# Optimization experiments

Hardware: AMD Instinct MI355X
Metric: run time of the kernel (lower is better)

Reference implementation:

```python
import jax, jax.numpy as jnp
import numpy as np

D_MODEL = 1024
NUM_HEADS = 16
HEAD_DIM = D_MODEL // NUM_HEADS


def setup_inputs() -> dict:
    key = jax.random.key(0)
    k_x, k_qkv, k_o = jax.random.split(key, 3)
    B, L = 2, 2048
    x = jax.random.normal(k_x, (B, L, D_MODEL), dtype=jnp.float32)
    # torch Linear weight [out, in]; y = x @ W.T. Scale ~ kaiming-uniform-ish.
    s = 1.0 / np.sqrt(D_MODEL)
    W_qkv = jax.random.uniform(k_qkv, (3 * D_MODEL, D_MODEL), dtype=jnp.float32, minval=-s, maxval=s)
    W_o = jax.random.uniform(k_o, (D_MODEL, D_MODEL), dtype=jnp.float32, minval=-s, maxval=s)
    return {"x": x, "W_qkv": W_qkv, "W_o": W_o}


def reference(x, W_qkv, W_o):
    B, L, D = x.shape
    H, dk = NUM_HEADS, HEAD_DIM
    qkv = (x @ W_qkv.T).reshape(B, L, 3, H, dk)
    q = qkv[:, :, 0].transpose(0, 2, 1, 3)  # [B,H,L,dk]
    k = qkv[:, :, 1].transpose(0, 2, 1, 3)
    v = qkv[:, :, 2].transpose(0, 2, 1, 3)
    scale = 1.0 / np.sqrt(dk).astype(np.float32)
    attn = jnp.einsum('bhqd,bhkd->bhqk', q, k) * scale  # [B,H,L,L]
    causal = jnp.tril(jnp.ones((L, L), dtype=bool))
    attn = jnp.where(causal, attn, -jnp.inf)
    attn = jax.nn.softmax(attn, axis=-1)
    y = jnp.einsum('bhqk,bhkd->bhqd', attn, v)  # [B,H,L,dk]
    y = y.transpose(0, 2, 1, 3).reshape(B, L, D)
    return y @ W_o.T
```

## Files before the change

kernel.cpp:

```cpp
#include <hip/hip_runtime.h>

typedef unsigned short u16;
typedef unsigned int   u32;

typedef __attribute__((ext_vector_type(4))) float  f32x4;
typedef __attribute__((ext_vector_type(8))) __bf16 bf16x8;

#define B_  2
#define L_  2048
#define H_  16

__device__ static inline u16 f2bf(float f) {
  u32 u = __builtin_bit_cast(u32, f);
  u32 r = u + 0x7fffu + ((u >> 16) & 1u);
  return (u16)(r >> 16);
}

__device__ static inline void gload_lds16(const u16* g, u16* lds) {
  __builtin_amdgcn_global_load_lds((__attribute__((address_space(1))) void*)(g),
                                   (__attribute__((address_space(3))) void*)(lds),
                                   16, 0, 0);
}

__global__ __launch_bounds__(256) void cvt3_kernel(
    const float4* __restrict__ a, uint2* __restrict__ ao, int na,
    const float4* __restrict__ b, uint2* __restrict__ bo, int nb,
    const float4* __restrict__ c, uint2* __restrict__ co, int nc)
{
  const int step = gridDim.x * 256;
  for (int i = blockIdx.x * 256 + threadIdx.x; i < na; i += step) {
    float4 f = a[i];
    ao[i] = make_uint2((u32)f2bf(f.x) | ((u32)f2bf(f.y) << 16),
                       (u32)f2bf(f.z) | ((u32)f2bf(f.w) << 16));
  }
  for (int i = blockIdx.x * 256 + threadIdx.x; i < nb; i += step) {
    float4 f = b[i];
    bo[i] = make_uint2((u32)f2bf(f.x) | ((u32)f2bf(f.y) << 16),
                       (u32)f2bf(f.z) | ((u32)f2bf(f.w) << 16));
  }
  for (int i = blockIdx.x * 256 + threadIdx.x; i < nc; i += step) {
    float4 f = c[i];
    co[i] = make_uint2((u32)f2bf(f.x) | ((u32)f2bf(f.y) << 16),
                       (u32)f2bf(f.z) | ((u32)f2bf(f.w) << 16));
  }
}

template <bool OUT_F32>
__global__ __launch_bounds__(256) void gemm_bt_kernel(
    const u16* __restrict__ A, const u16* __restrict__ Bt, void* __restrict__ Cv,
    const int K, const int N)
{
  __shared__ __attribute__((aligned(16))) u16 Al[128 * 64];
  __shared__ __attribute__((aligned(16))) u16 Bl[128 * 64];

  const int tid  = threadIdx.x;
  const int w    = tid >> 6;
  const int lane = tid & 63;
  const int m0 = blockIdx.y * 128;
  const int n0 = blockIdx.x * 128;
  const int mo = (w >> 1) * 64;
  const int no = (w & 1) * 64;

  const int srow = w * 32 + (lane >> 3);
  const int scol = (((lane & 7) ^ ((lane >> 3) & 7)) * 8);

  const f32x4 zero = {0.f, 0.f, 0.f, 0.f};
  f32x4 acc[4][4];
  #pragma unroll
  for (int i = 0; i < 4; ++i)
    #pragma unroll
    for (int j = 0; j < 4; ++j) acc[i][j] = zero;

  const int frow = lane & 15;
  const int fg   = lane >> 4;

  for (int k0 = 0; k0 < K; k0 += 64) {
    __syncthreads();
    #pragma unroll
    for (int inst = 0; inst < 4; ++inst) {
      const int r = srow + inst * 8;
      gload_lds16(A  + (size_t)(m0 + r) * K + k0 + scol, &Al[(w * 32 + inst * 8) * 64]);
      gload_lds16(Bt + (size_t)(n0 + r) * K + k0 + scol, &Bl[(w * 32 + inst * 8) * 64]);
    }
    __syncthreads();
    #pragma unroll
    for (int ks = 0; ks < 2; ++ks) {
      const int fco = ((ks * 4 + fg) ^ (frow & 7)) * 8;
      bf16x8 af[4], bfr[4];
      #pragma unroll
      for (int i = 0; i < 4; ++i)
        af[i] = *(const bf16x8*)&Al[(mo + i * 16 + frow) * 64 + fco];
      #pragma unroll
      for (int j = 0; j < 4; ++j)
        bfr[j] = *(const bf16x8*)&Bl[(no + j * 16 + frow) * 64 + fco];
      #pragma unroll
      for (int i = 0; i < 4; ++i)
        #pragma unroll
        for (int j = 0; j < 4; ++j)
          acc[i][j] = __builtin_amdgcn_mfma_f32_16x16x32_bf16(af[i], bfr[j], acc[i][j], 0, 0, 0);
    }
  }

  const int crow0 = m0 + mo + (lane >> 4) * 4;
  const int ccol0 = n0 + no + (lane & 15);
  #pragma unroll
  for (int i = 0; i < 4; ++i)
    #pragma unroll
    for (int j = 0; j < 4; ++j)
      #pragma unroll
      for (int r = 0; r < 4; ++r) {
        const size_t idx = (size_t)(crow0 + i * 16 + r) * N + (ccol0 + j * 16);
        if (OUT_F32) ((float*)Cv)[idx] = acc[i][j][r];
        else         ((u16*)Cv)[idx]   = f2bf(acc[i][j][r]);
      }
}

__global__ __launch_bounds__(256) void attn_mfma_kernel(const u16* __restrict__ qkv,
                                                        u16* __restrict__ y)
{
  __shared__ __attribute__((aligned(16))) u16 Kt[2][64 * 64];
  __shared__ __attribute__((aligned(16))) u16 Vt[2][64 * 72];
  __shared__ __attribute__((aligned(16))) u16 Pt[4][16 * 72];

  const int tid  = threadIdx.x;
  const int w    = tid >> 6;
  const int lane = tid & 63;
  const int fr   = lane & 15;
  const int fg   = lane >> 4;
  const int bh   = blockIdx.x;
  const int pi   = blockIdx.y;
  const int bb   = bh >> 4;
  const int hh   = bh & 15;
  const size_t rb = (size_t)bb * L_;

  const int vkk  = tid >> 2;
  const int vdb  = (tid & 3) * 16;
  const int vcol = vkk ^ ((tid & 3) * 16);

  const int pswz = (fr & 12) << 2;
  const int pfo0 = fr * 72 + ((fg * 8) ^ pswz);
  const int pfo1 = fr * 72 + ((32 + fg * 8) ^ pswz);

  const int ksr = w * 16 + (lane >> 3);
  const int ksc = (((lane & 7) ^ ((lane >> 3) & 7)) * 8);

  const int kco0 = ((fg) ^ (fr & 7)) * 8;
  const int kco1 = ((4 + fg) ^ (fr & 7)) * 8;

  const f32x4 zero = {0.f, 0.f, 0.f, 0.f};

  for (int pass = 0; pass < 2; ++pass) {
    const int qt = pass ? (31 - pi) : pi;
    const int q0 = qt * 64;
    const int qw = q0 + w * 16;

    const bf16x8 qf0 = *(const bf16x8*)(qkv + (rb + qw + fr) * 3072 + hh * 64 + fg * 8);
    const bf16x8 qf1 = *(const bf16x8*)(qkv + (rb + qw + fr) * 3072 + hh * 64 + 32 + fg * 8);

    f32x4 oacc[4];
    #pragma unroll
    for (int nt = 0; nt < 4; ++nt) oacc[nt] = zero;
    f32x4 lsum = zero;

    __syncthreads();
    #pragma unroll
    for (int inst = 0; inst < 2; ++inst)
      gload_lds16(qkv + (rb + 0 + ksr + inst * 8) * 3072 + 1024 + hh * 64 + ksc,
                  &Kt[0][(w * 16 + inst * 8) * 64]);
    {
      const u16* vp = qkv + (rb + 0 + vkk) * 3072 + 2048 + hh * 64 + vdb;
      uint4 a = *(const uint4*)vp;
      uint4 b = *(const uint4*)(vp + 8);
      u16 vals[16];
      *(uint4*)(vals)     = a;
      *(uint4*)(vals + 8) = b;
      #pragma unroll
      for (int i = 0; i < 16; ++i) Vt[0][(vdb + i) * 72 + vcol] = vals[i];
    }

    int cur = 0;
    for (int kt = 0; kt <= q0; kt += 64) {
      __syncthreads();

      const bool havenext = (kt + 64 <= q0);
      uint4 va, vb;
      if (havenext) {
        #pragma unroll
        for (int inst = 0; inst < 2; ++inst)
          gload_lds16(qkv + (rb + kt + 64 + ksr + inst * 8) * 3072 + 1024 + hh * 64 + ksc,
                      &Kt[cur ^ 1][(w * 16 + inst * 8) * 64]);
        const u16* vp = qkv + (rb + kt + 64 + vkk) * 3072 + 2048 + hh * 64 + vdb;
        va = *(const uint4*)vp;
        vb = *(const uint4*)(vp + 8);
      }

      f32x4 sacc[4];
      #pragma unroll
      for (int nt = 0; nt < 4; ++nt) sacc[nt] = zero;
      #pragma unroll
      for (int nt = 0; nt < 4; ++nt) {
        bf16x8 kf0 = *(const bf16x8*)&Kt[cur][(nt * 16 + fr) * 64 + kco0];
        sacc[nt] = __builtin_amdgcn_mfma_f32_16x16x32_bf16(qf0, kf0, sacc[nt], 0, 0, 0);
        bf16x8 kf1 = *(const bf16x8*)&Kt[cur][(nt * 16 + fr) * 64 + kco1];
        sacc[nt] = __builtin_amdgcn_mfma_f32_16x16x32_bf16(qf1, kf1, sacc[nt], 0, 0, 0);
      }

      if (kt == q0) {
        #pragma unroll
        for (int nt = 0; nt < 4; ++nt)
          #pragma unroll
          for (int r = 0; r < 4; ++r) {
            float p = (kt + nt * 16 + fr > qw + fg * 4 + r)
                          ? 0.f : __expf(sacc[nt][r] * 0.125f);
            lsum[r] += p;
            Pt[w][(fg * 4 + r) * 72 + ((nt * 16 + fr) ^ (fg * 16))] = f2bf(p);
          }
      } else {
        #pragma unroll
        for (int nt = 0; nt < 4; ++nt)
          #pragma unroll
          for (int r = 0; r < 4; ++r) {
            float p = __expf(sacc[nt][r] * 0.125f);
            lsum[r] += p;
            Pt[w][(fg * 4 + r) * 72 + ((nt * 16 + fr) ^ (fg * 16))] = f2bf(p);
          }
      }

      #pragma unroll
      for (int ks = 0; ks < 2; ++ks) {
        bf16x8 pf = *(const bf16x8*)&Pt[w][ks ? pfo1 : pfo0];
        #pragma unroll
        for (int nt = 0; nt < 4; ++nt) {
          bf16x8 vf = *(const bf16x8*)&Vt[cur][(nt * 16 + fr) * 72 + ((ks * 32 + fg * 8) ^ (nt * 16))];
          oacc[nt] = __builtin_amdgcn_mfma_f32_16x16x32_bf16(pf, vf, oacc[nt], 0, 0, 0);
        }
      }

      if (havenext) {
        u16 vals[16];
        *(uint4*)(vals)     = va;
        *(uint4*)(vals + 8) = vb;
        #pragma unroll
        for (int i = 0; i < 16; ++i) Vt[cur ^ 1][(vdb + i) * 72 + vcol] = vals[i];
      }
      cur ^= 1;
    }

    #pragma unroll
    for (int r = 0; r < 4; ++r) {
      float v = lsum[r];
      v += __shfl_xor(v, 1);
      v += __shfl_xor(v, 2);
      v += __shfl_xor(v, 4);
      v += __shfl_xor(v, 8);
      lsum[r] = 1.f / v;
    }

    #pragma unroll
    for (int nt = 0; nt < 4; ++nt)
      #pragma unroll
      for (int r = 0; r < 4; ++r)
        y[(rb + qw + fg * 4 + r) * 1024 + hh * 64 + nt * 16 + fr] =
            f2bf(oacc[nt][r] * lsum[r]);
  }
}

extern "C" void kernel_launch(void* const* d_in, const int* in_sizes, int n_in,
                              void* d_out, int out_size, void* d_ws, size_t ws_size,
                              hipStream_t stream)
{
  const float* x    = (const float*)d_in[0];
  const float* Wqkv = (const float*)d_in[1];
  const float* Wo   = (const float*)d_in[2];
  float* out = (float*)d_out;

  u16* xb    = (u16*)d_ws;
  u16* Wqkvb = xb    + (size_t)4096 * 1024;
  u16* Wob   = Wqkvb + (size_t)3072 * 1024;
  u16* qkv   = Wob   + (size_t)1024 * 1024;
  u16* y     = qkv   + (size_t)4096 * 3072;

  cvt3_kernel<<<dim3(2048), dim3(256), 0, stream>>>(
      (const float4*)x,    (uint2*)xb,    4096 * 1024 / 4,
      (const float4*)Wqkv, (uint2*)Wqkvb, 3072 * 1024 / 4,
      (const float4*)Wo,   (uint2*)Wob,   1024 * 1024 / 4);

  gemm_bt_kernel<false><<<dim3(3072 / 128, 4096 / 128), dim3(256), 0, stream>>>(
      xb, Wqkvb, qkv, 1024, 3072);
  attn_mfma_kernel<<<dim3(B_ * H_, 16), dim3(256), 0, stream>>>(qkv, y);
  gemm_bt_kernel<true><<<dim3(1024 / 128, 4096 / 128), dim3(256), 0, stream>>>(
      y, Wob, out, 1024, 1024);
}
```

Measured before the change: 185.1 us.

## Double-buffer GEMM LDS tiles and transpose attention MFMA layout for packed stores

The GEMM kernel now double-buffers its A/B LDS tiles, prefetching the next K-slice while computing the current one and dropping one barrier per iteration. The attention kernel swaps MFMA operand order so scores and outputs come out transposed. This lets P be written as packed 64-bit bf16 pairs, V be staged as packed key-pair dwords with a swizzle, the row sum be reduced with two shuffles instead of four per row, and the output be stored as vectorized 8-byte writes. The cost is doubled GEMM LDS use, which may lower occupancy.

Measured after the change: 188.7 us. Within noise of the previous version (+2.0%).

```diff
diff --git a/kernel.cpp b/kernel.cpp
--- a/kernel.cpp
+++ b/kernel.cpp
@@ -15,6 +15,9 @@
   u32 r = u + 0x7fffu + ((u >> 16) & 1u);
   return (u16)(r >> 16);
 }
+__device__ static inline u32 pack2(float a, float b) {
+  return (u32)f2bf(a) | ((u32)f2bf(b) << 16);
+}
 
 __device__ static inline void gload_lds16(const u16* g, u16* lds) {
   __builtin_amdgcn_global_load_lds((__attribute__((address_space(1))) void*)(g),
@@ -30,18 +33,15 @@
   const int step = gridDim.x * 256;
   for (int i = blockIdx.x * 256 + threadIdx.x; i < na; i += step) {
     float4 f = a[i];
-    ao[i] = make_uint2((u32)f2bf(f.x) | ((u32)f2bf(f.y) << 16),
-                       (u32)f2bf(f.z) | ((u32)f2bf(f.w) << 16));
+    ao[i] = make_uint2(pack2(f.x, f.y), pack2(f.z, f.w));
   }
   for (int i = blockIdx.x * 256 + threadIdx.x; i < nb; i += step) {
     float4 f = b[i];
-    bo[i] = make_uint2((u32)f2bf(f.x) | ((u32)f2bf(f.y) << 16),
-                       (u32)f2bf(f.z) | ((u32)f2bf(f.w) << 16));
+    bo[i] = make_uint2(pack2(f.x, f.y), pack2(f.z, f.w));
   }
   for (int i = blockIdx.x * 256 + threadIdx.x; i < nc; i += step) {
     float4 f = c[i];
-    co[i] = make_uint2((u32)f2bf(f.x) | ((u32)f2bf(f.y) << 16),
-                       (u32)f2bf(f.z) | ((u32)f2bf(f.w) << 16));
+    co[i] = make_uint2(pack2(f.x, f.y), pack2(f.z, f.w));
   }
 }
 
@@ -50,8 +50,8 @@
     const u16* __restrict__ A, const u16* __restrict__ Bt, void* __restrict__ Cv,
     const int K, const int N)
 {
-  __shared__ __attribute__((aligned(16))) u16 Al[128 * 64];
-  __shared__ __attribute__((aligned(16))) u16 Bl[128 * 64];
+  __shared__ __attribute__((aligned(16))) u16 Al[2][128 * 64];
+  __shared__ __attribute__((aligned(16))) u16 Bl[2][128 * 64];
 
   const int tid  = threadIdx.x;
   const int w    = tid >> 6;
@@ -74,31 +74,41 @@
   const int frow = lane & 15;
   const int fg   = lane >> 4;
 
+  #pragma unroll
+  for (int inst = 0; inst < 4; ++inst) {
+    const int r = srow + inst * 8;
+    gload_lds16(A  + (size_t)(m0 + r) * K + scol, &Al[0][(w * 32 + inst * 8) * 64]);
+    gload_lds16(Bt + (size_t)(n0 + r) * K + scol, &Bl[0][(w * 32 + inst * 8) * 64]);
+  }
+
+  int cur = 0;
   for (int k0 = 0; k0 < K; k0 += 64) {
     __syncthreads();
-    #pragma unroll
-    for (int inst = 0; inst < 4; ++inst) {
-      const int r = srow + inst * 8;
-      gload_lds16(A  + (size_t)(m0 + r) * K + k0 + scol, &Al[(w * 32 + inst * 8) * 64]);
-      gload_lds16(Bt + (size_t)(n0 + r) * K + k0 + scol, &Bl[(w * 32 + inst * 8) * 64]);
-    }
-    __syncthreads();
+    if (k0 + 64 < K) {
+      #pragma unroll
+      for (int inst = 0; inst < 4; ++inst) {
+        const int r = srow + inst * 8;
+        gload_lds16(A  + (size_t)(m0 + r) * K + k0 + 64 + scol, &Al[cur ^ 1][(w * 32 + inst * 8) * 64]);
+        gload_lds16(Bt + (size_t)(n0 + r) * K + k0 + 64 + scol, &Bl[cur ^ 1][(w * 32 + inst * 8) * 64]);
+      }
+    }
     #pragma unroll
     for (int ks = 0; ks < 2; ++ks) {
       const int fco = ((ks * 4 + fg) ^ (frow & 7)) * 8;
       bf16x8 af[4], bfr[4];
       #pragma unroll
       for (int i = 0; i < 4; ++i)
-        af[i] = *(const bf16x8*)&Al[(mo + i * 16 + frow) * 64 + fco];
+        af[i] = *(const bf16x8*)&Al[cur][(mo + i * 16 + frow) * 64 + fco];
       #pragma unroll
       for (int j = 0; j < 4; ++j)
-        bfr[j] = *(const bf16x8*)&Bl[(no + j * 16 + frow) * 64 + fco];
+        bfr[j] = *(const bf16x8*)&Bl[cur][(no + j * 16 + frow) * 64 + fco];
       #pragma unroll
       for (int i = 0; i < 4; ++i)
         #pragma unroll
         for (int j = 0; j < 4; ++j)
           acc[i][j] = __builtin_amdgcn_mfma_f32_16x16x32_bf16(af[i], bfr[j], acc[i][j], 0, 0, 0);
     }
+    cur ^= 1;
   }
 
   const int crow0 = m0 + mo + (lane >> 4) * 4;
@@ -119,8 +129,8 @@
                                                         u16* __restrict__ y)
 {
   __shared__ __attribute__((aligned(16))) u16 Kt[2][64 * 64];
-  __shared__ __attribute__((aligned(16))) u16 Vt[2][64 * 72];
-  __shared__ __attribute__((aligned(16))) u16 Pt[4][16 * 72];
+  __shared__ __attribute__((aligned(16))) u32 Vtd[2][64 * 40];
+  __shared__ __attribute__((aligned(16))) u32 PTd[4][16 * 40];
 
   const int tid  = threadIdx.x;
   const int w    = tid >> 6;
@@ -133,19 +143,15 @@
   const int hh   = bh & 15;
   const size_t rb = (size_t)bb * L_;
 
-  const int vkk  = tid >> 2;
-  const int vdb  = (tid & 3) * 16;
-  const int vcol = vkk ^ ((tid & 3) * 16);
-
-  const int pswz = (fr & 12) << 2;
-  const int pfo0 = fr * 72 + ((fg * 8) ^ pswz);
-  const int pfo1 = fr * 72 + ((32 + fg * 8) ^ pswz);
+  const int kkp = lane & 31;
+  const int dc  = 2 * w + (lane >> 5);
 
   const int ksr = w * 16 + (lane >> 3);
   const int ksc = (((lane & 7) ^ ((lane >> 3) & 7)) * 8);
-
   const int kco0 = ((fg) ^ (fr & 7)) * 8;
   const int kco1 = ((4 + fg) ^ (fr & 7)) * 8;
+
+  const int vro = 4 * (fg ^ (fr & 3));
 
   const f32x4 zero = {0.f, 0.f, 0.f, 0.f};
 
@@ -159,23 +165,23 @@
 
     f32x4 oacc[4];
     #pragma unroll
-    for (int nt = 0; nt < 4; ++nt) oacc[nt] = zero;
-    f32x4 lsum = zero;
+    for (int mt = 0; mt < 4; ++mt) oacc[mt] = zero;
+    float lsum = 0.f;
 
     __syncthreads();
     #pragma unroll
     for (int inst = 0; inst < 2; ++inst)
-      gload_lds16(qkv + (rb + 0 + ksr + inst * 8) * 3072 + 1024 + hh * 64 + ksc,
+      gload_lds16(qkv + (rb + ksr + inst * 8) * 3072 + 1024 + hh * 64 + ksc,
                   &Kt[0][(w * 16 + inst * 8) * 64]);
     {
-      const u16* vp = qkv + (rb + 0 + vkk) * 3072 + 2048 + hh * 64 + vdb;
-      uint4 a = *(const uint4*)vp;
-      uint4 b = *(const uint4*)(vp + 8);
-      u16 vals[16];
-      *(uint4*)(vals)     = a;
-      *(uint4*)(vals + 8) = b;
-      #pragma unroll
-      for (int i = 0; i < 16; ++i) Vt[0][(vdb + i) * 72 + vcol] = vals[i];
+      const u16* vp = qkv + (rb + 2 * kkp) * 3072 + 2048 + hh * 64 + dc * 8;
+      uint4 va = *(const uint4*)vp;
+      uint4 vb = *(const uint4*)(vp + 3072);
+      u16 a16[8], b16[8];
+      *(uint4*)a16 = va; *(uint4*)b16 = vb;
+      #pragma unroll
+      for (int i = 0; i < 8; ++i)
+        Vtd[0][(dc * 8 + i) * 40 + (kkp ^ (4 * (i & 3)))] = (u32)a16[i] | ((u32)b16[i] << 16);
     }
 
     int cur = 0;
@@ -189,9 +195,9 @@
         for (int inst = 0; inst < 2; ++inst)
           gload_lds16(qkv + (rb + kt + 64 + ksr + inst * 8) * 3072 + 1024 + hh * 64 + ksc,
                       &Kt[cur ^ 1][(w * 16 + inst * 8) * 64]);
-        const u16* vp = qkv + (rb + kt + 64 + vkk) * 3072 + 2048 + hh * 64 + vdb;
+        const u16* vp = qkv + (rb + kt + 64 + 2 * kkp) * 3072 + 2048 + hh * 64 + dc * 8;
         va = *(const uint4*)vp;
-        vb = *(const uint4*)(vp + 8);
+        vb = *(const uint4*)(vp + 3072);
       }
 
       f32x4 sacc[4];
@@ -200,68 +206,67 @@
       #pragma unroll
       for (int nt = 0; nt < 4; ++nt) {
         bf16x8 kf0 = *(const bf16x8*)&Kt[cur][(nt * 16 + fr) * 64 + kco0];
-        sacc[nt] = __builtin_amdgcn_mfma_f32_16x16x32_bf16(qf0, kf0, sacc[nt], 0, 0, 0);
+        sacc[nt] = __builtin_amdgcn_mfma_f32_16x16x32_bf16(kf0, qf0, sacc[nt], 0, 0, 0);
         bf16x8 kf1 = *(const bf16x8*)&Kt[cur][(nt * 16 + fr) * 64 + kco1];
-        sacc[nt] = __builtin_amdgcn_mfma_f32_16x16x32_bf16(qf1, kf1, sacc[nt], 0, 0, 0);
+        sacc[nt] = __builtin_amdgcn_mfma_f32_16x16x32_bf16(kf1, qf1, sacc[nt], 0, 0, 0);
       }
 
       if (kt == q0) {
         #pragma unroll
-        for (int nt = 0; nt < 4; ++nt)
+        for (int nt = 0; nt < 4; ++nt) {
+          float p[4];
           #pragma unroll
           for (int r = 0; r < 4; ++r) {
-            float p = (kt + nt * 16 + fr > qw + fg * 4 + r)
-                          ? 0.f : __expf(sacc[nt][r] * 0.125f);
-            lsum[r] += p;
-            Pt[w][(fg * 4 + r) * 72 + ((nt * 16 + fr) ^ (fg * 16))] = f2bf(p);
+            p[r] = (nt * 16 + 4 * fg + r > w * 16 + fr)
+                       ? 0.f : __expf(sacc[nt][r] * 0.125f);
+            lsum += p[r];
           }
+          *(uint2*)&PTd[w][fr * 40 + nt * 8 + 2 * fg] =
+              make_uint2(pack2(p[0], p[1]), pack2(p[2], p[3]));
+        }
       } else {
         #pragma unroll
-        for (int nt = 0; nt < 4; ++nt)
+        for (int nt = 0; nt < 4; ++nt) {
+          float p[4];
           #pragma unroll
           for (int r = 0; r < 4; ++r) {
-            float p = __expf(sacc[nt][r] * 0.125f);
-            lsum[r] += p;
-            Pt[w][(fg * 4 + r) * 72 + ((nt * 16 + fr) ^ (fg * 16))] = f2bf(p);
+            p[r] = __expf(sacc[nt][r] * 0.125f);
+            lsum += p[r];
           }
+          *(uint2*)&PTd[w][fr * 40 + nt * 8 + 2 * fg] =
+              make_uint2(pack2(p[0], p[1]), pack2(p[2], p[3]));
+        }
       }
 
       #pragma unroll
       for (int ks = 0; ks < 2; ++ks) {
-        bf16x8 pf = *(const bf16x8*)&Pt[w][ks ? pfo1 : pfo0];
-        #pragma unroll
-        for (int nt = 0; nt < 4; ++nt) {
-          bf16x8 vf = *(const bf16x8*)&Vt[cur][(nt * 16 + fr) * 72 + ((ks * 32 + fg * 8) ^ (nt * 16))];
-          oacc[nt] = __builtin_amdgcn_mfma_f32_16x16x32_bf16(pf, vf, oacc[nt], 0, 0, 0);
+        bf16x8 pf = *(const bf16x8*)&PTd[w][fr * 40 + ks * 16 + fg * 4];
+        #pragma unroll
+        for (int mt = 0; mt < 4; ++mt) {
+          bf16x8 vf = *(const bf16x8*)&Vtd[cur][(mt * 16 + fr) * 40 + ks * 16 + vro];
+          oacc[mt] = __builtin_amdgcn_mfma_f32_16x16x32_bf16(vf, pf, oacc[mt], 0, 0, 0);
         }
       }
 
       if (havenext) {
-        u16 vals[16];
-        *(uint4*)(vals)     = va;
-        *(uint4*)(vals + 8) = vb;
-        #pragma unroll
-        for (int i = 0; i < 16; ++i) Vt[cur ^ 1][(vdb + i) * 72 + vcol] = vals[i];
+        u16 a16[8], b16[8];
+        *(uint4*)a16 = va; *(uint4*)b16 = vb;
+        #pragma unroll
+        for (int i = 0; i < 8; ++i)
+          Vtd[cur ^ 1][(dc * 8 + i) * 40 + (kkp ^ (4 * (i & 3)))] = (u32)a16[i] | ((u32)b16[i] << 16);
       }
       cur ^= 1;
     }
 
-    #pragma unroll
-    for (int r = 0; r < 4; ++r) {
-      float v = lsum[r];
-      v += __shfl_xor(v, 1);
-      v += __shfl_xor(v, 2);
-      v += __shfl_xor(v, 4);
-      v += __shfl_xor(v, 8);
-      lsum[r] = 1.f / v;
-    }
-
-    #pragma unroll
-    for (int nt = 0; nt < 4; ++nt)
-      #pragma unroll
-      for (int r = 0; r < 4; ++r)
-        y[(rb + qw + fg * 4 + r) * 1024 + hh * 64 + nt * 16 + fr] =
-            f2bf(oacc[nt][r] * lsum[r]);
+    lsum += __shfl_xor(lsum, 16);
+    lsum += __shfl_xor(lsum, 32);
+    const float inv = 1.f / lsum;
+
+    u16* yp = y + (rb + qw + fr) * 1024 + hh * 64 + 4 * fg;
+    #pragma unroll
+    for (int mt = 0; mt < 4; ++mt)
+      *(uint2*)(yp + mt * 16) = make_uint2(pack2(oacc[mt][0] * inv, oacc[mt][1] * inv),
+                                           pack2(oacc[mt][2] * inv, oacc[mt][3] * inv));
   }
 }
 
```
